# Optimization experiments

Hardware: AMD Instinct MI355X
Metric: run time of the kernel (lower is better)

## Reference

```python
import jax, jax.numpy as jnp
import numpy as np

N_NODES = 100000
N_EDGES = 1600000
D_IN = 64
D_HID = 64
D_OUT = 64
DROP_P = 0.5


def _degree_norms(src, dst, n):
    ones = jnp.ones(src.shape[0], dtype=jnp.float32)
    deg_out = jax.ops.segment_sum(ones, src, num_segments=n)  # out-degree of src nodes
    deg_in = jax.ops.segment_sum(ones, dst, num_segments=n)   # in-degree of dst nodes
    norm_src = jnp.where(deg_out > 0, jax.lax.rsqrt(jnp.maximum(deg_out, 1.0)), 0.0)
    norm_dst = jnp.where(deg_in > 0, jax.lax.rsqrt(jnp.maximum(deg_in, 1.0)), 0.0)
    return norm_src, norm_dst


def _graph_conv(h, W, b, src, dst, norm_src, norm_dst, n, activation=None):
    # DGL GraphConv, norm='both': out = D_in^{-1/2} A (D_out^{-1/2} h) W + b
    h = h * norm_src[:, None]
    h = h @ W                      # small GEMM first (in >= out), math-equivalent
    msg = h[src]                   # gather  [E, d]
    agg = jax.ops.segment_sum(msg, dst, num_segments=n)  # scatter-add [N, d]
    out = agg * norm_dst[:, None] + b
    if activation is not None:
        out = activation(out)
    return out


def _dropout(h, key, p=DROP_P):
    keep = jax.random.bernoulli(key, 1.0 - p, h.shape)
    return jnp.where(keep, h / (1.0 - p), 0.0)


def setup_inputs() -> dict:
    key = jax.random.key(0)
    ks = jax.random.split(key, 6)
    x = jax.random.normal(ks[0], (N_NODES, D_IN), dtype=jnp.float32)
    W0 = jax.random.normal(ks[1], (D_IN, D_HID), dtype=jnp.float32) * 0.05
    W1 = jax.random.normal(ks[2], (D_HID, D_HID), dtype=jnp.float32) * 0.05
    W2 = jax.random.normal(ks[3], (D_HID, D_OUT), dtype=jnp.float32) * 0.05
    b0 = jnp.zeros((D_HID,), dtype=jnp.float32)
    b1 = jnp.zeros((D_HID,), dtype=jnp.float32)
    b2 = jnp.zeros((D_OUT,), dtype=jnp.float32)
    src = jax.random.randint(ks[4], (N_EDGES,), 0, N_NODES, dtype=jnp.int32)
    dst = jax.random.randint(ks[5], (N_EDGES,), 0, N_NODES, dtype=jnp.int32)
    return {"x": x, "W0": W0, "b0": b0, "W1": W1, "b1": b1, "W2": W2, "b2": b2,
            "src": src, "dst": dst}


def reference(x, W0, b0, W1, b1, W2, b2, src, dst):
    n = x.shape[0]
    norm_src, norm_dst = _degree_norms(src, dst, n)
    dk = jax.random.key(1)
    h = _graph_conv(x, W0, b0, src, dst, norm_src, norm_dst, n, jax.nn.relu)
    h = _dropout(h, jax.random.fold_in(dk, 0))
    h = _graph_conv(h, W1, b1, src, dst, norm_src, norm_dst, n, jax.nn.relu)
    h = _dropout(h, jax.random.fold_in(dk, 1))
    h = _graph_conv(h, W2, b2, src, dst, norm_src, norm_dst, n, None)
    return h
```

## Files before the change

kernel.cpp:

```cpp
#include <hip/hip_runtime.h>
#include <hip/hip_bf16.h>
#include <hip/hip_fp16.h>
#include <cstddef>


#define WG 256
#define WGB 512
#define WGD 1024
#define NWAVES (WGD / 64)
#define SLOT_S 48
#define NB_SHIFT 9
#define NB_W 512
#define EB 2048
#define PSTRIDE 257

__host__ __device__ static inline unsigned rotl32(unsigned x, int r) {
  return (x << r) | (x >> (32 - r));
}

__host__ __device__ static inline void threefry2x32(unsigned k0, unsigned k1,
                                                    unsigned x0, unsigned x1,
                                                    unsigned& o0, unsigned& o1) {
  unsigned ks2 = k0 ^ k1 ^ 0x1BD11BDAu;
  x0 += k0; x1 += k1;
#define TF_ROUND(r) { x0 += x1; x1 = rotl32(x1, r); x1 ^= x0; }
  TF_ROUND(13) TF_ROUND(15) TF_ROUND(26) TF_ROUND(6)
  x0 += k1;  x1 += ks2 + 1u;
  TF_ROUND(17) TF_ROUND(29) TF_ROUND(16) TF_ROUND(24)
  x0 += ks2; x1 += k0 + 2u;
  TF_ROUND(13) TF_ROUND(15) TF_ROUND(26) TF_ROUND(6)
  x0 += k0;  x1 += k1 + 3u;
  TF_ROUND(17) TF_ROUND(29) TF_ROUND(16) TF_ROUND(24)
  x0 += k1;  x1 += ks2 + 4u;
  TF_ROUND(13) TF_ROUND(15) TF_ROUND(26) TF_ROUND(6)
  x0 += ks2; x1 += k0 + 5u;
#undef TF_ROUND
  o0 = x0; o1 = x1;
}

__device__ static inline float2 h2f(unsigned u) {
  return __half22float2(__builtin_bit_cast(__half2, u));
}
__device__ static inline unsigned f2h(float a, float b) {
  return __builtin_bit_cast(unsigned, __floats2half2_rn(a, b));
}


__global__ __launch_bounds__(WGB) void bin_k(
    const int* __restrict__ src, const int* __restrict__ dst,
    unsigned* __restrict__ binbuf_d, unsigned short* __restrict__ binbuf_s,
    unsigned short* __restrict__ pref_d, unsigned short* __restrict__ pref_s,
    int e) {
  __shared__ int hist_d[256], hist_s[256];
  __shared__ int scan_d[256], scan_s[256];
  __shared__ int curs_d[256], curs_s[256];
  __shared__ unsigned sorted_d[EB];
  __shared__ unsigned short sorted_s[EB];
  int tid = threadIdx.x;
  int blk = blockIdx.x;
  int base = blk * EB;
  int cnt = e - base;
  if (cnt > EB) cnt = EB;

  if (tid < 256) { hist_d[tid] = 0; hist_s[tid] = 0; }
  __syncthreads();
  for (int i = tid; i < cnt; i += WGB) {
    int d = dst[base + i];
    int s = src[base + i];
    atomicAdd(&hist_d[d >> NB_SHIFT], 1);
    atomicAdd(&hist_s[s >> NB_SHIFT], 1);
  }
  __syncthreads();
  int hd = 0, hs = 0;
  if (tid < 256) {
    hd = hist_d[tid]; hs = hist_s[tid];
    scan_d[tid] = hd;
    scan_s[tid] = hs;
  }
  __syncthreads();
  for (int st = 1; st < 256; st <<= 1) {
    int ad = 0, as = 0;
    if (tid < 256 && tid >= st) { ad = scan_d[tid - st]; as = scan_s[tid - st]; }
    __syncthreads();
    if (tid < 256) { scan_d[tid] += ad; scan_s[tid] += as; }
    __syncthreads();
  }
  if (tid < 256) {
    int ed = scan_d[tid] - hd;
    int es = scan_s[tid] - hs;
    curs_d[tid] = ed;
    curs_s[tid] = es;
    pref_d[(size_t)blk * PSTRIDE + tid] = (unsigned short)ed;
    pref_s[(size_t)blk * PSTRIDE + tid] = (unsigned short)es;
    if (tid == 255) {
      pref_d[(size_t)blk * PSTRIDE + 256] = (unsigned short)scan_d[255];
      pref_s[(size_t)blk * PSTRIDE + 256] = (unsigned short)scan_s[255];
    }
  }
  __syncthreads();
  for (int i = tid; i < cnt; i += WGB) {
    int d = dst[base + i];
    int s = src[base + i];
    int pd = atomicAdd(&curs_d[d >> NB_SHIFT], 1);
    sorted_d[pd] = ((unsigned)(d & (NB_W - 1)) << 17) | (unsigned)s;
    int ps = atomicAdd(&curs_s[s >> NB_SHIFT], 1);
    sorted_s[ps] = (unsigned short)(s & (NB_W - 1));
  }
  __syncthreads();
  for (int i = tid; i < cnt; i += WGB) binbuf_d[base + i] = sorted_d[i];
  for (int i = tid; i < cnt; i += WGB) binbuf_s[base + i] = sorted_s[i];
}


__global__ __launch_bounds__(WGD) void debin_k(
    const unsigned* __restrict__ binbuf_d,
    const unsigned short* __restrict__ binbuf_s,
    const unsigned short* __restrict__ pref_d,
    const unsigned short* __restrict__ pref_s,
    int* __restrict__ slot, int* __restrict__ cnt_in,
    float* __restrict__ nsrc, int n, int nblk, int nwg) {
  __shared__ int lcnt[NB_W];
  int tid = threadIdx.x;
  int wave = tid >> 6;
  int lane = tid & 63;

  int j = blockIdx.x;
  int q = nwg >> 3, r = nwg & 7;
  int x = j & 7, p = j >> 3;
  int vb = (x < r ? x * (q + 1) : r * (q + 1) + (x - r) * q) + p;
  int role = vb & 1;
  int b = vb >> 1;

  for (int i = tid; i < NB_W; i += WGD) lcnt[i] = 0;
  __syncthreads();

  if (role == 0) {
    for (int seg = wave; seg < nblk; seg += NWAVES) {
      const unsigned short* pr = pref_d + (size_t)seg * PSTRIDE + b;
      int p0 = pr[0], p1 = pr[1];
      const unsigned* bb = binbuf_d + (size_t)seg * EB;
      for (int i = p0 + lane; i < p1; i += 64) {
        unsigned v = bb[i];
        int dl = v >> 17;
        int s = (int)(v & 0x1FFFFu);
        int c = atomicAdd(&lcnt[dl], 1);
        if (c < SLOT_S) slot[(size_t)((b << NB_SHIFT) + dl) * SLOT_S + c] = s;
      }
    }
    __syncthreads();
    for (int i = tid; i < NB_W; i += WGD) {
      int v = (b << NB_SHIFT) + i;
      if (v < n) cnt_in[v] = lcnt[i];
    }
  } else {
    for (int seg = wave; seg < nblk; seg += NWAVES) {
      const unsigned short* pr = pref_s + (size_t)seg * PSTRIDE + b;
      int p0 = pr[0], p1 = pr[1];
      const unsigned short* bb = binbuf_s + (size_t)seg * EB;
      for (int i = p0 + lane; i < p1; i += 64) atomicAdd(&lcnt[bb[i]], 1);
    }
    __syncthreads();
    int vbase = b << NB_SHIFT;
    for (int i = tid; i < NB_W; i += WGD) {
      int v = vbase + i;
      if (v < n) {
        int c = lcnt[i];
        nsrc[v] = (c > 0) ? rsqrtf((float)c) : 0.f;
      }
    }
  }
}


__global__ __launch_bounds__(WG) void ns_k(
    const float* __restrict__ nsrc, const float* __restrict__ x,
    unsigned short* __restrict__ G0, int n) {
  int idx = blockIdx.x * WG + threadIdx.x;
  int v = idx >> 4;
  if (v >= n) return;
  float ns = nsrc[v];
  float4 rr = ((const float4*)x)[(size_t)v * 16 + (idx & 15)];
  ((uint2*)G0)[(size_t)v * 16 + (idx & 15)] =
      make_uint2(f2h(rr.x * ns, rr.y * ns), f2h(rr.z * ns, rr.w * ns));
}

__global__ __launch_bounds__(WG) void layer_k(
    const unsigned short* __restrict__ G, const int* __restrict__ slot,
    const int* __restrict__ cnt_in, const float* __restrict__ nsrc,
    const float* __restrict__ W, const float* __restrict__ bias,
    unsigned short* __restrict__ GoutH, float* __restrict__ GoutF,
    int n, int mid, unsigned dk0, unsigned dk1) {
  __shared__ float4 Ws[1024];
  __shared__ __align__(16) float rows[4][272];
  const float4* W4 = (const float4*)W;
  for (int i = threadIdx.x; i < 1024; i += WG) Ws[i] = W4[i];

  int wave = threadIdx.x >> 6;
  int lane = threadIdx.x & 63;
  int g = lane >> 4;
  int l16 = lane & 15;
  int v = blockIdx.x * 16 + wave * 4 + g;
  bool valid = (v < n);
  int vc = valid ? v : (n - 1);

  int degt = valid ? cnt_in[vc] : 0;
  int deg = (degt > SLOT_S) ? SLOT_S : degt;
  const int* sl = slot + (size_t)vc * SLOT_S;
  const uint2* G2 = (const uint2*)G;

  float4 aA = make_float4(0.f, 0.f, 0.f, 0.f);
  float4 aB = make_float4(0.f, 0.f, 0.f, 0.f);
  float4 aC = make_float4(0.f, 0.f, 0.f, 0.f);
  float4 aD = make_float4(0.f, 0.f, 0.f, 0.f);
#define ACC(dst, m) { float2 lo = h2f((m).x), hi = h2f((m).y); \
    dst.x += lo.x; dst.y += lo.y; dst.z += hi.x; dst.w += hi.y; }
  int nq = deg >> 2;
  int i = 0;
  for (; i + 1 < nq; i += 2) {
    int4 q0 = *(const int4*)(sl + i * 4);
    int4 q1 = *(const int4*)(sl + i * 4 + 4);
    uint2 m0 = G2[(size_t)q0.x * 16 + l16];
    uint2 m1 = G2[(size_t)q0.y * 16 + l16];
    uint2 m2 = G2[(size_t)q0.z * 16 + l16];
    uint2 m3 = G2[(size_t)q0.w * 16 + l16];
    uint2 m4 = G2[(size_t)q1.x * 16 + l16];
    uint2 m5 = G2[(size_t)q1.y * 16 + l16];
    uint2 m6 = G2[(size_t)q1.z * 16 + l16];
    uint2 m7 = G2[(size_t)q1.w * 16 + l16];
    ACC(aA, m0) ACC(aB, m1) ACC(aC, m2) ACC(aD, m3)
    ACC(aA, m4) ACC(aB, m5) ACC(aC, m6) ACC(aD, m7)
  }
  if (i < nq) {
    int4 q0 = *(const int4*)(sl + i * 4);
    uint2 m0 = G2[(size_t)q0.x * 16 + l16];
    uint2 m1 = G2[(size_t)q0.y * 16 + l16];
    uint2 m2 = G2[(size_t)q0.z * 16 + l16];
    uint2 m3 = G2[(size_t)q0.w * 16 + l16];
    ACC(aA, m0) ACC(aB, m1) ACC(aC, m2) ACC(aD, m3)
  }
  int rem = deg & 3;
  if (rem) {
    int4 q = *(const int4*)(sl + (deg & ~3));
    int s0 = q.x;
    int s1 = (rem > 1) ? q.y : s0;
    int s2 = (rem > 2) ? q.z : s0;
    float w1 = (rem > 1) ? 1.f : 0.f;
    float w2 = (rem > 2) ? 1.f : 0.f;
    uint2 m0 = G2[(size_t)s0 * 16 + l16];
    uint2 m1 = G2[(size_t)s1 * 16 + l16];
    uint2 m2 = G2[(size_t)s2 * 16 + l16];
    ACC(aA, m0)
    { float2 lo = h2f(m1.x), hi = h2f(m1.y);
      aB.x = fmaf(w1, lo.x, aB.x); aB.y = fmaf(w1, lo.y, aB.y);
      aB.z = fmaf(w1, hi.x, aB.z); aB.w = fmaf(w1, hi.y, aB.w); }
    { float2 lo = h2f(m2.x), hi = h2f(m2.y);
      aC.x = fmaf(w2, lo.x, aC.x); aC.y = fmaf(w2, lo.y, aC.y);
      aC.z = fmaf(w2, hi.x, aC.z); aC.w = fmaf(w2, hi.y, aC.w); }
  }
#undef ACC
  float4 agg;
  agg.x = (aA.x + aB.x) + (aC.x + aD.x);
  agg.y = (aA.y + aB.y) + (aC.y + aD.y);
  agg.z = (aA.z + aB.z) + (aC.z + aD.z);
  agg.w = (aA.w + aB.w) + (aC.w + aD.w);

  float* rw = &rows[wave][g * 68];
  *(float4*)(rw + l16 * 4) = agg;
  __syncthreads();

  float4 acc = make_float4(0.f, 0.f, 0.f, 0.f);
#pragma unroll
  for (int k = 0; k < 64; ++k) {
    float a = rw[k];
    float4 w = Ws[k * 16 + l16];
    acc.x = fmaf(a, w.x, acc.x);
    acc.y = fmaf(a, w.y, acc.y);
    acc.z = fmaf(a, w.z, acc.z);
    acc.w = fmaf(a, w.w, acc.w);
  }

  float nd = (degt > 0) ? rsqrtf((float)degt) : 0.f;
  float4 b4 = ((const float4*)bias)[l16];
  float4 o;
  o.x = fmaf(acc.x, nd, b4.x);
  o.y = fmaf(acc.y, nd, b4.y);
  o.z = fmaf(acc.z, nd, b4.z);
  o.w = fmaf(acc.w, nd, b4.w);
  if (mid) {
    o.x = fmaxf(o.x, 0.f); o.y = fmaxf(o.y, 0.f);
    o.z = fmaxf(o.z, 0.f); o.w = fmaxf(o.w, 0.f);
    unsigned idx = (unsigned)(v * 64 + l16 * 4);
    unsigned r0a, r0b, r1a, r1b, r2a, r2b, r3a, r3b;
    threefry2x32(dk0, dk1, 0u, idx + 0u, r0a, r0b);
    threefry2x32(dk0, dk1, 0u, idx + 1u, r1a, r1b);
    threefry2x32(dk0, dk1, 0u, idx + 2u, r2a, r2b);
    threefry2x32(dk0, dk1, 0u, idx + 3u, r3a, r3b);
    float ns2 = 2.f * nsrc[vc];
    o.x = ((r0a ^ r0b) & 0x80000000u) ? 0.f : o.x * ns2;
    o.y = ((r1a ^ r1b) & 0x80000000u) ? 0.f : o.y * ns2;
    o.z = ((r2a ^ r2b) & 0x80000000u) ? 0.f : o.z * ns2;
    o.w = ((r3a ^ r3b) & 0x80000000u) ? 0.f : o.w * ns2;
    if (valid)
      ((uint2*)GoutH)[(size_t)v * 16 + l16] =
          make_uint2(f2h(o.x, o.y), f2h(o.z, o.w));
  } else {
    if (valid) ((float4*)GoutF)[(size_t)v * 16 + l16] = o;
  }
}


extern "C" void kernel_launch(void* const* d_in, const int* in_sizes, int n_in,
                              void* d_out, int out_size, void* d_ws, size_t ws_size,
                              hipStream_t stream) {
  const float* x  = (const float*)d_in[0];
  const float* W0 = (const float*)d_in[1];
  const float* b0 = (const float*)d_in[2];
  const float* W1 = (const float*)d_in[3];
  const float* b1 = (const float*)d_in[4];
  const float* W2 = (const float*)d_in[5];
  const float* b2 = (const float*)d_in[6];
  const int* src  = (const int*)d_in[7];
  const int* dst  = (const int*)d_in[8];
  float* out = (float*)d_out;

  const int n = in_sizes[0] / 64;
  const int e = in_sizes[7];
  const int nbuck = (n + NB_W - 1) / NB_W;
  const int nblk = (e + EB - 1) / EB;

  char* w = (char*)d_ws;
  size_t off = 0;
  auto alloc = [&](size_t bytes) -> void* {
    void* p = w + off;
    off += (bytes + 255) & ~(size_t)255;
    return p;
  };
  int*            cnt_in   = (int*)alloc((size_t)n * 4);
  float*          nsrc     = (float*)alloc((size_t)n * 4);
  unsigned*       binbuf_d = (unsigned*)alloc((size_t)nblk * EB * 4);
  unsigned short* binbuf_s = (unsigned short*)alloc((size_t)nblk * EB * 2);
  unsigned short* pref_d   = (unsigned short*)alloc((size_t)nblk * PSTRIDE * 2);
  unsigned short* pref_s   = (unsigned short*)alloc((size_t)nblk * PSTRIDE * 2);
  int*            slot     = (int*)alloc((size_t)nbuck * NB_W * SLOT_S * 4);
  unsigned short* G0       = (unsigned short*)alloc((size_t)n * 64 * 2);
  unsigned short* G1       = (unsigned short*)alloc((size_t)n * 64 * 2);

  unsigned k0a, k0b, k1a, k1b;
  threefry2x32(0u, 1u, 0u, 0u, k0a, k0b);
  threefry2x32(0u, 1u, 0u, 1u, k1a, k1b);

  const int gL = (n + 15) / 16;
  const int gN = (n * 16 + WG - 1) / WG;

  bin_k<<<nblk, WGB, 0, stream>>>(src, dst, binbuf_d, binbuf_s,
                                  pref_d, pref_s, e);
  debin_k<<<2 * nbuck, WGD, 0, stream>>>(binbuf_d, binbuf_s, pref_d, pref_s,
                                         slot, cnt_in, nsrc, n, nblk,
                                         2 * nbuck);
  ns_k<<<gN, WG, 0, stream>>>(nsrc, x, G0, n);

  layer_k<<<gL, WG, 0, stream>>>(G0, slot, cnt_in, nsrc, W0, b0, G1, nullptr,
                                 n, 1, k0a, k0b);
  layer_k<<<gL, WG, 0, stream>>>(G1, slot, cnt_in, nsrc, W1, b1, G0, nullptr,
                                 n, 1, k1a, k1b);
  layer_k<<<gL, WG, 0, stream>>>(G0, slot, cnt_in, nsrc, W2, b2, nullptr, out,
                                 n, 0, 0u, 0u);
}
```

Measured before the change: 280.4 us.

## Precompute dropout bitmasks in debin kernel and enlarge layer workgroups

Both layers' dropout masks are now generated with threefry inside the atomic-bound debin kernel, packed as bits, and interleaved with the binning work across waves. The mid layers then read one mask word per thread instead of running four threefry hashes each. The layer kernel workgroup also grows from 256 to 512 threads (32 nodes per block). This adds a small mask buffer and extra work to debin, in exchange for less ALU work on the layer critical path.

```diff
diff --git a/kernel.cpp b/kernel.cpp
--- a/kernel.cpp
+++ b/kernel.cpp
@@ -5,6 +5,7 @@
 
 
 #define WG 256
+#define WGL 512
 #define WGB 512
 #define WGD 1024
 #define NWAVES (WGD / 64)
@@ -118,7 +119,9 @@
     const unsigned short* __restrict__ pref_d,
     const unsigned short* __restrict__ pref_s,
     int* __restrict__ slot, int* __restrict__ cnt_in,
-    float* __restrict__ nsrc, int n, int nblk, int nwg) {
+    float* __restrict__ nsrc, unsigned* __restrict__ mask,
+    int n, int nblk, int nwg,
+    unsigned mk0a, unsigned mk0b, unsigned mk1a, unsigned mk1b) {
   __shared__ int lcnt[NB_W];
   int tid = threadIdx.x;
   int wave = tid >> 6;
@@ -131,8 +134,30 @@
   int role = vb & 1;
   int b = vb >> 1;
 
+  int t = blockIdx.x * WGD + tid;
+  int w2 = 2 * n;
+  auto gen_mask = [&]() {
+    if (t < 2 * w2) {
+      int layer1 = (t >= w2) ? 1 : 0;
+      unsigned k0 = layer1 ? mk1a : mk0a;
+      unsigned k1 = layer1 ? mk1b : mk0b;
+      unsigned base = (unsigned)(t - layer1 * w2) * 32u;
+      unsigned m = 0;
+#pragma unroll 2
+      for (int jj = 0; jj < 32; ++jj) {
+        unsigned a, bb;
+        threefry2x32(k0, k1, 0u, base + (unsigned)jj, a, bb);
+        m |= ((a ^ bb) >> 31) << jj;
+      }
+      mask[t] = m;
+    }
+  };
+
   for (int i = tid; i < NB_W; i += WGD) lcnt[i] = 0;
   __syncthreads();
+
+  bool mask_first = (wave & 1) == 0;
+  if (mask_first) gen_mask();
 
   if (role == 0) {
     for (int seg = wave; seg < nblk; seg += NWAVES) {
@@ -169,6 +194,8 @@
       }
     }
   }
+
+  if (!mask_first) gen_mask();
 }
 
 
@@ -184,22 +211,23 @@
       make_uint2(f2h(rr.x * ns, rr.y * ns), f2h(rr.z * ns, rr.w * ns));
 }
 
-__global__ __launch_bounds__(WG) void layer_k(
+__global__ __launch_bounds__(WGL) void layer_k(
     const unsigned short* __restrict__ G, const int* __restrict__ slot,
     const int* __restrict__ cnt_in, const float* __restrict__ nsrc,
     const float* __restrict__ W, const float* __restrict__ bias,
+    const unsigned* __restrict__ mask,
     unsigned short* __restrict__ GoutH, float* __restrict__ GoutF,
-    int n, int mid, unsigned dk0, unsigned dk1) {
+    int n, int mid) {
   __shared__ float4 Ws[1024];
-  __shared__ __align__(16) float rows[4][272];
+  __shared__ __align__(16) float rows[8][272];
   const float4* W4 = (const float4*)W;
-  for (int i = threadIdx.x; i < 1024; i += WG) Ws[i] = W4[i];
+  for (int i = threadIdx.x; i < 1024; i += WGL) Ws[i] = W4[i];
 
   int wave = threadIdx.x >> 6;
   int lane = threadIdx.x & 63;
   int g = lane >> 4;
   int l16 = lane & 15;
-  int v = blockIdx.x * 16 + wave * 4 + g;
+  int v = blockIdx.x * 32 + wave * 4 + g;
   bool valid = (v < n);
   int vc = valid ? v : (n - 1);
 
@@ -289,17 +317,13 @@
   if (mid) {
     o.x = fmaxf(o.x, 0.f); o.y = fmaxf(o.y, 0.f);
     o.z = fmaxf(o.z, 0.f); o.w = fmaxf(o.w, 0.f);
-    unsigned idx = (unsigned)(v * 64 + l16 * 4);
-    unsigned r0a, r0b, r1a, r1b, r2a, r2b, r3a, r3b;
-    threefry2x32(dk0, dk1, 0u, idx + 0u, r0a, r0b);
-    threefry2x32(dk0, dk1, 0u, idx + 1u, r1a, r1b);
-    threefry2x32(dk0, dk1, 0u, idx + 2u, r2a, r2b);
-    threefry2x32(dk0, dk1, 0u, idx + 3u, r3a, r3b);
+    unsigned mword = mask[((size_t)vc << 1) + (l16 >> 3)];
+    unsigned sh = (unsigned)(l16 & 7) * 4u;
     float ns2 = 2.f * nsrc[vc];
-    o.x = ((r0a ^ r0b) & 0x80000000u) ? 0.f : o.x * ns2;
-    o.y = ((r1a ^ r1b) & 0x80000000u) ? 0.f : o.y * ns2;
-    o.z = ((r2a ^ r2b) & 0x80000000u) ? 0.f : o.z * ns2;
-    o.w = ((r3a ^ r3b) & 0x80000000u) ? 0.f : o.w * ns2;
+    o.x = ((mword >> (sh + 0u)) & 1u) ? 0.f : o.x * ns2;
+    o.y = ((mword >> (sh + 1u)) & 1u) ? 0.f : o.y * ns2;
+    o.z = ((mword >> (sh + 2u)) & 1u) ? 0.f : o.z * ns2;
+    o.w = ((mword >> (sh + 3u)) & 1u) ? 0.f : o.w * ns2;
     if (valid)
       ((uint2*)GoutH)[(size_t)v * 16 + l16] =
           make_uint2(f2h(o.x, o.y), f2h(o.z, o.w));
@@ -337,6 +361,7 @@
   };
   int*            cnt_in   = (int*)alloc((size_t)n * 4);
   float*          nsrc     = (float*)alloc((size_t)n * 4);
+  unsigned*       maskbuf  = (unsigned*)alloc((size_t)4 * n * 4);
   unsigned*       binbuf_d = (unsigned*)alloc((size_t)nblk * EB * 4);
   unsigned short* binbuf_s = (unsigned short*)alloc((size_t)nblk * EB * 2);
   unsigned short* pref_d   = (unsigned short*)alloc((size_t)nblk * PSTRIDE * 2);
@@ -349,20 +374,21 @@
   threefry2x32(0u, 1u, 0u, 0u, k0a, k0b);
   threefry2x32(0u, 1u, 0u, 1u, k1a, k1b);
 
-  const int gL = (n + 15) / 16;
+  const int gL = (n + 31) / 32;
   const int gN = (n * 16 + WG - 1) / WG;
 
   bin_k<<<nblk, WGB, 0, stream>>>(src, dst, binbuf_d, binbuf_s,
                                   pref_d, pref_s, e);
   debin_k<<<2 * nbuck, WGD, 0, stream>>>(binbuf_d, binbuf_s, pref_d, pref_s,
-                                         slot, cnt_in, nsrc, n, nblk,
-                                         2 * nbuck);
+                                         slot, cnt_in, nsrc, maskbuf,
+                                         n, nblk, 2 * nbuck,
+                                         k0a, k0b, k1a, k1b);
   ns_k<<<gN, WG, 0, stream>>>(nsrc, x, G0, n);
 
-  layer_k<<<gL, WG, 0, stream>>>(G0, slot, cnt_in, nsrc, W0, b0, G1, nullptr,
-                                 n, 1, k0a, k0b);
-  layer_k<<<gL, WG, 0, stream>>>(G1, slot, cnt_in, nsrc, W1, b1, G0, nullptr,
-                                 n, 1, k1a, k1b);
-  layer_k<<<gL, WG, 0, stream>>>(G0, slot, cnt_in, nsrc, W2, b2, nullptr, out,
-                                 n, 0, 0u, 0u);
-}
+  layer_k<<<gL, WGL, 0, stream>>>(G0, slot, cnt_in, nsrc, W0, b0,
+                                  maskbuf, G1, nullptr, n, 1);
+  layer_k<<<gL, WGL, 0, stream>>>(G1, slot, cnt_in, nsrc, W1, b1,
+                                  maskbuf + (size_t)2 * n, G0, nullptr, n, 1);
+  layer_k<<<gL, WGL, 0, stream>>>(G0, slot, cnt_in, nsrc, W2, b2,
+                                  nullptr, nullptr, out, n, 0);
+}
```

Result: slower. 325.1 us (+16.0%).

## Fuse source-norm scaling into debin and enlarge binning blocks with vector loads

Applied to the files above, without the earlier changes.

Removes the separate ns_k kernel by having the source-degree role of debin_k scale x by the freshly computed norm and write the half-precision G0 directly. bin_k now processes 4096 edges per 1024-thread block and reads src and dst with int4 vector loads. This saves one launch and a re-read of nsrc, and halves the number of bin segments that debin scans. In exchange, the fused role blocks do more serial work, and each bin block uses more shared memory, since the sorted buffers double in size.

```diff
diff --git a/kernel.cpp b/kernel.cpp
--- a/kernel.cpp
+++ b/kernel.cpp
@@ -5,13 +5,13 @@
 
 
 #define WG 256
-#define WGB 512
+#define WGB 1024
 #define WGD 1024
 #define NWAVES (WGD / 64)
 #define SLOT_S 48
 #define NB_SHIFT 9
 #define NB_W 512
-#define EB 2048
+#define EB 4096
 #define PSTRIDE 257
 
 __host__ __device__ static inline unsigned rotl32(unsigned x, int r) {
@@ -64,11 +64,22 @@
 
   if (tid < 256) { hist_d[tid] = 0; hist_s[tid] = 0; }
   __syncthreads();
-  for (int i = tid; i < cnt; i += WGB) {
-    int d = dst[base + i];
-    int s = src[base + i];
-    atomicAdd(&hist_d[d >> NB_SHIFT], 1);
-    atomicAdd(&hist_s[s >> NB_SHIFT], 1);
+  int cnt4 = cnt & ~3;
+  for (int i = tid * 4; i < cnt4; i += WGB * 4) {
+    int4 d4 = *(const int4*)(dst + base + i);
+    int4 s4 = *(const int4*)(src + base + i);
+    atomicAdd(&hist_d[d4.x >> NB_SHIFT], 1);
+    atomicAdd(&hist_d[d4.y >> NB_SHIFT], 1);
+    atomicAdd(&hist_d[d4.z >> NB_SHIFT], 1);
+    atomicAdd(&hist_d[d4.w >> NB_SHIFT], 1);
+    atomicAdd(&hist_s[s4.x >> NB_SHIFT], 1);
+    atomicAdd(&hist_s[s4.y >> NB_SHIFT], 1);
+    atomicAdd(&hist_s[s4.z >> NB_SHIFT], 1);
+    atomicAdd(&hist_s[s4.w >> NB_SHIFT], 1);
+  }
+  for (int i = cnt4 + tid; i < cnt; i += WGB) {
+    atomicAdd(&hist_d[dst[base + i] >> NB_SHIFT], 1);
+    atomicAdd(&hist_s[src[base + i] >> NB_SHIFT], 1);
   }
   __syncthreads();
   int hd = 0, hs = 0;
@@ -98,14 +109,22 @@
     }
   }
   __syncthreads();
-  for (int i = tid; i < cnt; i += WGB) {
+  for (int i = tid * 4; i < cnt4; i += WGB * 4) {
+    int4 d4 = *(const int4*)(dst + base + i);
+    int4 s4 = *(const int4*)(src + base + i);
+#define BIN1(dd, ss) { \
+    int pd = atomicAdd(&curs_d[(dd) >> NB_SHIFT], 1); \
+    sorted_d[pd] = ((unsigned)((dd) & (NB_W - 1)) << 17) | (unsigned)(ss); \
+    int ps = atomicAdd(&curs_s[(ss) >> NB_SHIFT], 1); \
+    sorted_s[ps] = (unsigned short)((ss) & (NB_W - 1)); }
+    BIN1(d4.x, s4.x) BIN1(d4.y, s4.y) BIN1(d4.z, s4.z) BIN1(d4.w, s4.w)
+  }
+  for (int i = cnt4 + tid; i < cnt; i += WGB) {
     int d = dst[base + i];
     int s = src[base + i];
-    int pd = atomicAdd(&curs_d[d >> NB_SHIFT], 1);
-    sorted_d[pd] = ((unsigned)(d & (NB_W - 1)) << 17) | (unsigned)s;
-    int ps = atomicAdd(&curs_s[s >> NB_SHIFT], 1);
-    sorted_s[ps] = (unsigned short)(s & (NB_W - 1));
-  }
+    BIN1(d, s)
+  }
+#undef BIN1
   __syncthreads();
   for (int i = tid; i < cnt; i += WGB) binbuf_d[base + i] = sorted_d[i];
   for (int i = tid; i < cnt; i += WGB) binbuf_s[base + i] = sorted_s[i];
@@ -118,16 +137,18 @@
     const unsigned short* __restrict__ pref_d,
     const unsigned short* __restrict__ pref_s,
     int* __restrict__ slot, int* __restrict__ cnt_in,
-    float* __restrict__ nsrc, int n, int nblk, int nwg) {
+    float* __restrict__ nsrc, const float* __restrict__ x,
+    unsigned short* __restrict__ G0, int n, int nblk, int nwg) {
   __shared__ int lcnt[NB_W];
+  __shared__ float lns[NB_W];
   int tid = threadIdx.x;
   int wave = tid >> 6;
   int lane = tid & 63;
 
   int j = blockIdx.x;
   int q = nwg >> 3, r = nwg & 7;
-  int x = j & 7, p = j >> 3;
-  int vb = (x < r ? x * (q + 1) : r * (q + 1) + (x - r) * q) + p;
+  int x8 = j & 7, p = j >> 3;
+  int vb = (x8 < r ? x8 * (q + 1) : r * (q + 1) + (x8 - r) * q) + p;
   int role = vb & 1;
   int b = vb >> 1;
 
@@ -165,23 +186,26 @@
       int v = vbase + i;
       if (v < n) {
         int c = lcnt[i];
-        nsrc[v] = (c > 0) ? rsqrtf((float)c) : 0.f;
+        float ns = (c > 0) ? rsqrtf((float)c) : 0.f;
+        lns[i] = ns;
+        nsrc[v] = ns;
       }
     }
-  }
-}
-
-
-__global__ __launch_bounds__(WG) void ns_k(
-    const float* __restrict__ nsrc, const float* __restrict__ x,
-    unsigned short* __restrict__ G0, int n) {
-  int idx = blockIdx.x * WG + threadIdx.x;
-  int v = idx >> 4;
-  if (v >= n) return;
-  float ns = nsrc[v];
-  float4 rr = ((const float4*)x)[(size_t)v * 16 + (idx & 15)];
-  ((uint2*)G0)[(size_t)v * 16 + (idx & 15)] =
-      make_uint2(f2h(rr.x * ns, rr.y * ns), f2h(rr.z * ns, rr.w * ns));
+    __syncthreads();
+    const float4* x4 = (const float4*)x;
+    uint2* G2 = (uint2*)G0;
+    int lim = NB_W * 16;
+    for (int idx = tid; idx < lim; idx += WGD) {
+      int nl = idx >> 4;
+      int v = vbase + nl;
+      if (v < n) {
+        float ns = lns[nl];
+        float4 rr = x4[(size_t)v * 16 + (idx & 15)];
+        G2[(size_t)v * 16 + (idx & 15)] =
+            make_uint2(f2h(rr.x * ns, rr.y * ns), f2h(rr.z * ns, rr.w * ns));
+      }
+    }
+  }
 }
 
 __global__ __launch_bounds__(WG) void layer_k(
@@ -240,10 +264,10 @@
   }
   int rem = deg & 3;
   if (rem) {
-    int4 q = *(const int4*)(sl + (deg & ~3));
-    int s0 = q.x;
-    int s1 = (rem > 1) ? q.y : s0;
-    int s2 = (rem > 2) ? q.z : s0;
+    int4 qq = *(const int4*)(sl + (deg & ~3));
+    int s0 = qq.x;
+    int s1 = (rem > 1) ? qq.y : s0;
+    int s2 = (rem > 2) ? qq.z : s0;
     float w1 = (rem > 1) ? 1.f : 0.f;
     float w2 = (rem > 2) ? 1.f : 0.f;
     uint2 m0 = G2[(size_t)s0 * 16 + l16];
@@ -350,14 +374,12 @@
   threefry2x32(0u, 1u, 0u, 1u, k1a, k1b);
 
   const int gL = (n + 15) / 16;
-  const int gN = (n * 16 + WG - 1) / WG;
 
   bin_k<<<nblk, WGB, 0, stream>>>(src, dst, binbuf_d, binbuf_s,
                                   pref_d, pref_s, e);
   debin_k<<<2 * nbuck, WGD, 0, stream>>>(binbuf_d, binbuf_s, pref_d, pref_s,
-                                         slot, cnt_in, nsrc, n, nblk,
-                                         2 * nbuck);
-  ns_k<<<gN, WG, 0, stream>>>(nsrc, x, G0, n);
+                                         slot, cnt_in, nsrc, x, G0,
+                                         n, nblk, 2 * nbuck);
 
   layer_k<<<gL, WG, 0, stream>>>(G0, slot, cnt_in, nsrc, W0, b0, G1, nullptr,
                                  n, 1, k0a, k0b);
```

After: 266.0 us. 1.05x faster.
